# Kernel tuning notes

Hardware: AMD Instinct MI355X
Metric: run time of the kernel (lower is better)

Reference implementation:

```python
import jax, jax.numpy as jnp
import numpy as np

B, T, F = 32, 2048, 16
C = F + 1      # input channels (time prepended)
H = 64         # output_dims: latent CDE state size
HH = 64        # hidden_dims: vector-field MLP width
DEPTH = 4      # num_hidden_layers -> DEPTH-1 inner linears
INIT = 64      # intial_dims


def _lin(k, fan_in, shape):
    b = 1.0 / np.sqrt(fan_in)
    return jax.random.uniform(k, shape, jnp.float32, -b, b)


def setup_inputs() -> dict:
    key = jax.random.key(0)
    ks = jax.random.split(key, 15)
    return {
        "x": jax.random.normal(ks[0], (B, T, F), jnp.float32),
        # z0 initializer MLP: Linear(C,INIT) -> ReLU -> Linear(INIT,H)
        "wi1": _lin(ks[1], C, (C, INIT)), "bi1": _lin(ks[2], C, (INIT,)),
        "wi2": _lin(ks[3], INIT, (INIT, H)), "bi2": _lin(ks[4], INIT, (H,)),
        # CDEFunc
        "w_in": _lin(ks[5], H, (H, HH)), "b_in": _lin(ks[6], H, (HH,)),
        "w_hid": _lin(ks[7], HH, (DEPTH - 1, HH, HH)), "b_hid": _lin(ks[8], HH, (DEPTH - 1, HH)),
        "w_out": _lin(ks[9], HH, (HH, C * H)), "b_out": _lin(ks[10], HH, (C * H,)),
        # output projection Linear(H, F)
        "w_proj": _lin(ks[11], H, (H, F)), "b_proj": _lin(ks[12], H, (F,)),
    }


def _cde_f(z, w_in, b_in, w_hid, b_hid, w_out, b_out):
    # CDEFunc.forward: MLP -> tanh, reshaped to (b, H, C)
    h = jax.nn.relu(z @ w_in + b_in)
    for i in range(w_hid.shape[0]):
        h = jax.nn.relu(h @ w_hid[i] + b_hid[i])
    return jnp.tanh((h @ w_out + b_out).reshape(z.shape[0], H, C))


def _forward(x, wi1, bi1, wi2, bi2, w_in, b_in, w_hid, b_hid, w_out, b_out, w_proj, b_proj):
    b, t_len, _ = x.shape
    t = jnp.arange(t_len, dtype=x.dtype)
    xa = jnp.concatenate([jnp.broadcast_to(t[None, :, None], (b, t_len, 1)), x], axis=-1)  # (b,T,C)

    # Hermite cubic with backward differences (torchcde): knot derivs are backward
    # diffs with the first repeated; on interval i (h=1):
    #   X'(s) = d_i + 2*c_i*s + 3*e_i*s^2,  c_i = 3*dx - 2*d_i - d_{i+1},  e_i = -2*dx + d_i + d_{i+1}
    diffs = xa[:, 1:] - xa[:, :-1]                      # (b,T-1,C)
    d = jnp.concatenate([diffs[:, :1], diffs], axis=1)  # (b,T,C)
    di, dip1 = d[:, :-1], d[:, 1:]
    cc = 3.0 * diffs - 2.0 * di - dip1
    ee = -2.0 * diffs + di + dip1

    def deriv(s):
        return di + (2.0 * s) * cc + (3.0 * s * s) * ee  # (b,T-1,C)

    # torchdiffeq 'rk4' = 3/8-rule: evals at s = 0, 1/3, 2/3, 1 within each unit interval
    xdots = jnp.stack([deriv(0.0), deriv(1.0 / 3.0), deriv(2.0 / 3.0), deriv(1.0)], axis=0)
    xdots = jnp.moveaxis(xdots, 2, 0)  # (T-1, 4, b, C)

    z0 = jax.nn.relu(xa[:, 0] @ wi1 + bi1) @ wi2 + bi2  # (b,H)

    def g(z, xd):
        f = _cde_f(z, w_in, b_in, w_hid, b_hid, w_out, b_out)  # (b,H,C)
        return jnp.einsum('bhc,bc->bh', f, xd)

    def step(z, xd4):
        k1 = g(z, xd4[0])
        k2 = g(z + k1 / 3.0, xd4[1])
        k3 = g(z + (k2 - k1 / 3.0), xd4[2])
        k4 = g(z + (k1 - k2 + k3), xd4[3])
        zn = z + (k1 + 3.0 * (k2 + k3) + k4) * 0.125
        return zn, zn

    _, zs = jax.lax.scan(step, z0, xdots)                # (T-1,b,H)
    z_T = jnp.moveaxis(jnp.concatenate([z0[None], zs], axis=0), 0, 1)  # (b,T,H)

    # act -> dropout (eval: identity) -> output_layer
    out = jax.nn.gelu(z_T, approximate=False) @ w_proj + b_proj        # (b,T,F)
    return z_T, out


def reference(x, wi1, bi1, wi2, bi2, w_in, b_in, w_hid, b_hid, w_out, b_out, w_proj, b_proj):
    z_T, out = _forward(x, wi1, bi1, wi2, bi2, w_in, b_in, w_hid, b_hid, w_out, b_out, w_proj, b_proj)
    not_mask = jnp.zeros((x.shape[0], x.shape[1]), dtype=bool)  # mask='all_true' (eval mode)
    return z_T, out, not_mask
```

## Files before the change

### kernel.cpp

```cpp
#include <hip/hip_runtime.h>
#include <math.h>

#define BB 32
#define TT 2048
#define FF 16
#define CC 17
#define HH 64

typedef float v2f __attribute__((ext_vector_type(2)));
typedef float v4f __attribute__((ext_vector_type(4)));
typedef unsigned int v4u __attribute__((ext_vector_type(4)));
typedef _Float16 h2 __attribute__((ext_vector_type(2)));

__device__ __forceinline__ float rl(float v, int lane) {
    return __int_as_float(__builtin_amdgcn_readlane(__float_as_int(v), lane));
}
__device__ __forceinline__ float uf(float v) {
    return __int_as_float(__builtin_amdgcn_readfirstlane(__float_as_int(v)));
}
__device__ __forceinline__ float ftanh(float x) {
    float e = __builtin_amdgcn_exp2f(x * 2.88539008177792681472f);
    return 1.0f - 2.0f * __builtin_amdgcn_rcpf(e + 1.0f);
}
__device__ __forceinline__ float fdot2(unsigned int a, unsigned int b, float c) {
    h2 ha = __builtin_bit_cast(h2, a), hb = __builtin_bit_cast(h2, b);
#if __has_builtin(__builtin_amdgcn_fdot2)
    return __builtin_amdgcn_fdot2(ha, hb, c, false);
#else
    return fmaf((float)ha.x, (float)hb.x, fmaf((float)ha.y, (float)hb.y, c));
#endif
}
__device__ __forceinline__ unsigned int packf16(float a, float b) {
    h2 p; p.x = (_Float16)a; p.y = (_Float16)b;
    return __builtin_bit_cast(unsigned int, p);
}

#define PIN(v) asm volatile("" : "+v"(v))

__attribute__((amdgpu_waves_per_eu(2, 2)))
__launch_bounds__(512)
__global__ void ncde_main(const float* __restrict__ x,
                          const float* __restrict__ wi1, const float* __restrict__ bi1,
                          const float* __restrict__ wi2, const float* __restrict__ bi2,
                          const float* __restrict__ w_in, const float* __restrict__ b_in,
                          const float* __restrict__ w_hid, const float* __restrict__ b_hid,
                          const float* __restrict__ w_out, const float* __restrict__ b_out,
                          float* __restrict__ zT)
{
    const int b   = blockIdx.x;
    const int tid = threadIdx.x;
    const int w   = tid >> 6;
    const int l   = tid & 63;

    __shared__ float Wl[4][64][64];
    __shared__ float ph[4][8][64];
    __shared__ __align__(16) unsigned int hb16[32];
    __shared__ v2f  pgq[8][64];

    {
        float* wl = (float*)Wl;
        for (int i = tid; i < 64 * 64; i += 512)     wl[i] = w_in[i];
        for (int i = tid; i < 3 * 64 * 64; i += 512) wl[64 * 64 + i] = w_hid[i];
    }

    float bfold[4];
    bfold[0] = (w == 0) ? b_in[l] : 0.0f;
    bfold[1] = (w == 0) ? b_hid[0 * HH + l] : 0.0f;
    bfold[2] = (w == 0) ? b_hid[1 * HH + l] : 0.0f;
    bfold[3] = (w == 0) ? b_hid[2 * HH + l] : 0.0f;

    const int c0 = 2 * w, c1 = 2 * w + 1;
    unsigned int wo0p[32], wo1p[32], w16p[4];
    #pragma unroll
    for (int j = 0; j < 32; ++j) {
        wo0p[j] = packf16(w_out[(2 * j) * (CC * HH) + l * CC + c0],
                          w_out[(2 * j + 1) * (CC * HH) + l * CC + c0]);
        wo1p[j] = packf16(w_out[(2 * j) * (CC * HH) + l * CC + c1],
                          w_out[(2 * j + 1) * (CC * HH) + l * CC + c1]);
    }
    #pragma unroll
    for (int j = 0; j < 4; ++j)
        w16p[j] = packf16(w_out[(8 * w + 2 * j) * (CC * HH) + l * CC + 16],
                          w_out[(8 * w + 2 * j + 1) * (CC * HH) + l * CC + 16]);
    float bo0  = b_out[l * CC + c0];
    float bo1  = b_out[l * CC + c1];
    float bo16 = b_out[l * CC + 16];

    #pragma unroll
    for (int j = 0; j < 32; ++j) { PIN(wo0p[j]); PIN(wo1p[j]); }
    #pragma unroll
    for (int j = 0; j < 4; ++j) PIN(w16p[j]);

    __syncthreads();

    float h0 = bi1[l];
    #pragma unroll
    for (int c = 1; c < CC; ++c) {
        float xc = x[(b * TT + 0) * FF + (c - 1)];
        h0 = fmaf(xc, wi1[c * HH + l], h0);
    }
    h0 = fmaxf(h0, 0.0f);
    float z = bi2[l];
    #pragma unroll
    for (int k = 0; k < 64; ++k)
        z = fmaf(rl(h0, k), wi2[k * HH + l], z);

    if (w == 0) zT[(b * TT + 0) * HH + l] = z;

    auto G = [&](float zin, float xd0, float xd1, float xd16) -> float {
        float cur = zin;
        #pragma unroll
        for (int layer = 0; layer < 4; ++layer) {
            float wk0 = Wl[layer][8 * w + 0][l], wk1 = Wl[layer][8 * w + 1][l];
            float wk2 = Wl[layer][8 * w + 2][l], wk3 = Wl[layer][8 * w + 3][l];
            float wk4 = Wl[layer][8 * w + 4][l], wk5 = Wl[layer][8 * w + 5][l];
            float wk6 = Wl[layer][8 * w + 6][l], wk7 = Wl[layer][8 * w + 7][l];
            float a0 = bfold[layer], a1 = 0.0f;
            a0 = fmaf(rl(cur, 8 * w + 0), wk0, a0);
            a1 = fmaf(rl(cur, 8 * w + 1), wk1, a1);
            a0 = fmaf(rl(cur, 8 * w + 2), wk2, a0);
            a1 = fmaf(rl(cur, 8 * w + 3), wk3, a1);
            a0 = fmaf(rl(cur, 8 * w + 4), wk4, a0);
            a1 = fmaf(rl(cur, 8 * w + 5), wk5, a1);
            a0 = fmaf(rl(cur, 8 * w + 6), wk6, a0);
            a1 = fmaf(rl(cur, 8 * w + 7), wk7, a1);
            ph[layer][w][l] = a0 + a1;
            __syncthreads();
            float r0 = ph[layer][0][l], r1 = ph[layer][1][l];
            float r2 = ph[layer][2][l], r3 = ph[layer][3][l];
            float r4 = ph[layer][4][l], r5 = ph[layer][5][l];
            float r6 = ph[layer][6][l], r7 = ph[layer][7][l];
            cur = fmaxf(((r0 + r1) + (r2 + r3)) + ((r4 + r5) + (r6 + r7)), 0.0f);
        }
        float pm = __shfl_xor(cur, 1);
        if (w == 0 && (l & 1) == 0)
            hb16[l >> 1] = __builtin_bit_cast(unsigned int,
                __builtin_amdgcn_cvt_pkrtz(cur * 0.00390625f, pm * 0.00390625f));
        __syncthreads();

        float u0a = 0.f, u0b = 0.f, u0c = 0.f, u0d = 0.f;
        float u1a = 0.f, u1b = 0.f, u1c = 0.f, u1d = 0.f;
        #pragma unroll
        for (int j = 0; j < 8; ++j) {
            v4u q = *reinterpret_cast<const v4u*>(&hb16[4 * j]);
            u0a = fdot2(q.x, wo0p[4 * j + 0], u0a);
            u0b = fdot2(q.y, wo0p[4 * j + 1], u0b);
            u0c = fdot2(q.z, wo0p[4 * j + 2], u0c);
            u0d = fdot2(q.w, wo0p[4 * j + 3], u0d);
            u1a = fdot2(q.x, wo1p[4 * j + 0], u1a);
            u1b = fdot2(q.y, wo1p[4 * j + 1], u1b);
            u1c = fdot2(q.z, wo1p[4 * j + 2], u1c);
            u1d = fdot2(q.w, wo1p[4 * j + 3], u1d);
        }
        float u0 = fmaf(((u0a + u0b) + (u0c + u0d)), 256.0f, bo0);
        float u1 = fmaf(((u1a + u1b) + (u1c + u1d)), 256.0f, bo1);

        v4u qc = *reinterpret_cast<const v4u*>(&hb16[4 * w]);
        float a16a = fdot2(qc.x, w16p[0], 0.0f);
        float a16b = fdot2(qc.y, w16p[1], 0.0f);
        a16a = fdot2(qc.z, w16p[2], a16a);
        a16b = fdot2(qc.w, w16p[3], a16b);

        float pg = ftanh(u0) * xd0 + ftanh(u1) * xd1;
        pgq[w][l] = (v2f){ pg, a16a + a16b };
        __syncthreads();
        v2f s0 = pgq[0][l], s1 = pgq[1][l], s2 = pgq[2][l], s3 = pgq[3][l];
        v2f s4 = pgq[4][l], s5 = pgq[5][l], s6 = pgq[6][l], s7 = pgq[7][l];
        v2f st = ((s0 + s1) + (s2 + s3)) + ((s4 + s5) + (s6 + s7));
        float u16 = fmaf(st.y, 256.0f, bo16);
        return fmaf(ftanh(u16), xd16, st.x);
    };

    const float* xb = x + (size_t)b * TT * FF;
    const bool hasc0 = (w != 0);
    const int  f0 = 2 * w - 1;
    const int  f1 = 2 * w;
    float xp0  = hasc0 ? uf(xb[0 * FF + f0]) : 0.0f;
    float xp1  = uf(xb[0 * FF + f1]);
    float xp16 = uf(xb[0 * FF + 15]);
    float xn0  = hasc0 ? uf(xb[1 * FF + f0]) : 0.0f;
    float xn1  = uf(xb[1 * FF + f1]);
    float xn16 = uf(xb[1 * FF + 15]);
    float dc0  = hasc0 ? (xn0 - xp0) : 1.0f;
    float dc1  = xn1 - xp1;
    float dc16 = xn16 - xp16;
    float dp0 = dc0, dp1 = dc1, dp16 = dc16;
    xp0 = xn0; xp1 = xn1; xp16 = xn16;

    #pragma unroll 1
    for (int t = 0; t < TT - 1; ++t) {
        const float f43 = 4.0f / 3.0f;
        float x20  = dp0  + f43 * (dc0  - dp0);
        float x21  = dp1  + f43 * (dc1  - dp1);
        float x216 = dp16 + f43 * (dc16 - dp16);

        int tn = (t + 2 < TT) ? (t + 2) : (TT - 1);
        float yn0  = hasc0 ? uf(xb[tn * FF + f0]) : 0.0f;
        float yn1  = uf(xb[tn * FF + f1]);
        float yn16 = uf(xb[tn * FF + 15]);

        float k1 = G(z, dp0, dp1, dp16);
        float k2 = G(z + k1 * (1.0f / 3.0f), dc0, dc1, dc16);
        float k3 = G(z + (k2 - k1 * (1.0f / 3.0f)), x20, x21, x216);
        float k4 = G(z + (k1 - k2 + k3), dc0, dc1, dc16);
        z = z + 0.125f * (k1 + 3.0f * (k2 + k3) + k4);

        if (w == 0) zT[(b * TT + (t + 1)) * HH + l] = z;

        dp0 = dc0; dp1 = dc1; dp16 = dc16;
        dc0 = hasc0 ? (yn0 - xp0) : 1.0f;
        dc1 = yn1 - xp1;
        dc16 = yn16 - xp16;
        xp0 = yn0; xp1 = yn1; xp16 = yn16;
    }
}

__global__ void ncde_proj(const float* __restrict__ zT,
                          const float* __restrict__ w_proj, const float* __restrict__ b_proj,
                          float* __restrict__ out, float* __restrict__ mask)
{
    __shared__ float gz[16][64];
    const int blk = blockIdx.x;
    const int tid = threadIdx.x;
    const int r16 = tid >> 4, f = tid & 15;
    const int row0 = blk * 16;

    #pragma unroll
    for (int i = 0; i < 4; ++i) {
        int idx = tid + i * 256;
        int r = idx >> 6, k = idx & 63;
        float zv = zT[(size_t)(row0 + r) * HH + k];
        gz[r][k] = 0.5f * zv * (1.0f + erff(zv * 0.70710678118654752f));
    }
    __syncthreads();

    float acc = b_proj[f];
    #pragma unroll
    for (int k = 0; k < 64; ++k)
        acc = fmaf(gz[r16][k], w_proj[k * FF + f], acc);
    out[(size_t)(row0 + r16) * FF + f] = acc;
    if (f == 0) mask[row0 + r16] = 0.0f;
}

extern "C" void kernel_launch(void* const* d_in, const int* in_sizes, int n_in,
                              void* d_out, int out_size, void* d_ws, size_t ws_size,
                              hipStream_t stream)
{
    (void)in_sizes; (void)n_in; (void)d_ws; (void)ws_size; (void)out_size;
    const float* x      = (const float*)d_in[0];
    const float* wi1    = (const float*)d_in[1];
    const float* bi1    = (const float*)d_in[2];
    const float* wi2    = (const float*)d_in[3];
    const float* bi2    = (const float*)d_in[4];
    const float* w_in   = (const float*)d_in[5];
    const float* b_in   = (const float*)d_in[6];
    const float* w_hid  = (const float*)d_in[7];
    const float* b_hid  = (const float*)d_in[8];
    const float* w_out  = (const float*)d_in[9];
    const float* b_out  = (const float*)d_in[10];
    const float* w_proj = (const float*)d_in[11];
    const float* b_proj = (const float*)d_in[12];

    float* zT   = (float*)d_out;
    float* outp = zT + (size_t)BB * TT * HH;
    float* mask = outp + (size_t)BB * TT * FF;

    ncde_main<<<dim3(BB), dim3(512), 0, stream>>>(
        x, wi1, bi1, wi2, bi2, w_in, b_in, w_hid, b_hid, w_out, b_out, zT);
    ncde_proj<<<dim3((BB * TT) / 16), dim3(256), 0, stream>>>(
        zT, w_proj, b_proj, outp, mask);
}
```

Before: 14.31 ms.

## Process two batch elements per block to amortize barriers and latency

Each workgroup now integrates two independent batch sequences at once, so the grid is halved. LDS partial-sum buffers are widened so both sequences share each barrier. A lighter barrier that only waits on LDS counters replaces __syncthreads. The aim is to fill the latency and synchronisation stalls of the serial RK4 chain with independent work, at the cost of more registers and half as many active CUs.

New measurement: 21.58 ms. +50.8%, slower.

```diff
diff --git a/kernel.cpp b/kernel.cpp
--- a/kernel.cpp
+++ b/kernel.cpp
@@ -24,21 +24,18 @@
 }
 __device__ __forceinline__ float fdot2(unsigned int a, unsigned int b, float c) {
     h2 ha = __builtin_bit_cast(h2, a), hb = __builtin_bit_cast(h2, b);
-#if __has_builtin(__builtin_amdgcn_fdot2)
     return __builtin_amdgcn_fdot2(ha, hb, c, false);
-#else
-    return fmaf((float)ha.x, (float)hb.x, fmaf((float)ha.y, (float)hb.y, c));
-#endif
 }
 __device__ __forceinline__ unsigned int packf16(float a, float b) {
     h2 p; p.x = (_Float16)a; p.y = (_Float16)b;
     return __builtin_bit_cast(unsigned int, p);
 }
-
+__device__ __forceinline__ void bar_lds() {
+    asm volatile("s_waitcnt lgkmcnt(0)\n\ts_barrier" ::: "memory");
+}
 #define PIN(v) asm volatile("" : "+v"(v))
 
-__attribute__((amdgpu_waves_per_eu(2, 2)))
-__launch_bounds__(512)
+__launch_bounds__(512, 2)
 __global__ void ncde_main(const float* __restrict__ x,
                           const float* __restrict__ wi1, const float* __restrict__ bi1,
                           const float* __restrict__ wi2, const float* __restrict__ bi2,
@@ -47,15 +44,16 @@
                           const float* __restrict__ w_out, const float* __restrict__ b_out,
                           float* __restrict__ zT)
 {
-    const int b   = blockIdx.x;
+    const int bid = blockIdx.x;
+    const int eA = 2 * bid, eB = 2 * bid + 1;
     const int tid = threadIdx.x;
     const int w   = tid >> 6;
     const int l   = tid & 63;
 
     __shared__ float Wl[4][64][64];
-    __shared__ float ph[4][8][64];
-    __shared__ __align__(16) unsigned int hb16[32];
-    __shared__ v2f  pgq[8][64];
+    __shared__ v2f  ph[4][8][64];
+    __shared__ __align__(16) unsigned int hb16[64];
+    __shared__ v4f  pgq[8][64];
 
     {
         float* wl = (float*)Wl;
@@ -93,125 +91,171 @@
 
     __syncthreads();
 
-    float h0 = bi1[l];
-    #pragma unroll
-    for (int c = 1; c < CC; ++c) {
-        float xc = x[(b * TT + 0) * FF + (c - 1)];
-        h0 = fmaf(xc, wi1[c * HH + l], h0);
-    }
-    h0 = fmaxf(h0, 0.0f);
-    float z = bi2[l];
-    #pragma unroll
-    for (int k = 0; k < 64; ++k)
-        z = fmaf(rl(h0, k), wi2[k * HH + l], z);
-
-    if (w == 0) zT[(b * TT + 0) * HH + l] = z;
-
-    auto G = [&](float zin, float xd0, float xd1, float xd16) -> float {
-        float cur = zin;
+    float zA, zB;
+    {
+        float h0A = bi1[l], h0B = bi1[l];
+        #pragma unroll
+        for (int c = 1; c < CC; ++c) {
+            float w1 = wi1[c * HH + l];
+            h0A = fmaf(x[(size_t)eA * TT * FF + (c - 1)], w1, h0A);
+            h0B = fmaf(x[(size_t)eB * TT * FF + (c - 1)], w1, h0B);
+        }
+        h0A = fmaxf(h0A, 0.0f); h0B = fmaxf(h0B, 0.0f);
+        zA = bi2[l]; zB = zA;
+        #pragma unroll
+        for (int k = 0; k < 64; ++k) {
+            float w2 = wi2[k * HH + l];
+            zA = fmaf(rl(h0A, k), w2, zA);
+            zB = fmaf(rl(h0B, k), w2, zB);
+        }
+    }
+    if (w == 0) {
+        zT[(size_t)eA * TT * HH + l] = zA;
+        zT[(size_t)eB * TT * HH + l] = zB;
+    }
+
+    auto G2 = [&](float ziA, float ziB,
+                  float xa0, float xa1, float xa16,
+                  float xb0, float xb1, float xb16) -> v2f {
+        float cA = ziA, cB = ziB;
         #pragma unroll
         for (int layer = 0; layer < 4; ++layer) {
-            float wk0 = Wl[layer][8 * w + 0][l], wk1 = Wl[layer][8 * w + 1][l];
-            float wk2 = Wl[layer][8 * w + 2][l], wk3 = Wl[layer][8 * w + 3][l];
-            float wk4 = Wl[layer][8 * w + 4][l], wk5 = Wl[layer][8 * w + 5][l];
-            float wk6 = Wl[layer][8 * w + 6][l], wk7 = Wl[layer][8 * w + 7][l];
-            float a0 = bfold[layer], a1 = 0.0f;
-            a0 = fmaf(rl(cur, 8 * w + 0), wk0, a0);
-            a1 = fmaf(rl(cur, 8 * w + 1), wk1, a1);
-            a0 = fmaf(rl(cur, 8 * w + 2), wk2, a0);
-            a1 = fmaf(rl(cur, 8 * w + 3), wk3, a1);
-            a0 = fmaf(rl(cur, 8 * w + 4), wk4, a0);
-            a1 = fmaf(rl(cur, 8 * w + 5), wk5, a1);
-            a0 = fmaf(rl(cur, 8 * w + 6), wk6, a0);
-            a1 = fmaf(rl(cur, 8 * w + 7), wk7, a1);
-            ph[layer][w][l] = a0 + a1;
-            __syncthreads();
-            float r0 = ph[layer][0][l], r1 = ph[layer][1][l];
-            float r2 = ph[layer][2][l], r3 = ph[layer][3][l];
-            float r4 = ph[layer][4][l], r5 = ph[layer][5][l];
-            float r6 = ph[layer][6][l], r7 = ph[layer][7][l];
-            cur = fmaxf(((r0 + r1) + (r2 + r3)) + ((r4 + r5) + (r6 + r7)), 0.0f);
-        }
-        float pm = __shfl_xor(cur, 1);
-        if (w == 0 && (l & 1) == 0)
+            float pA  = bfold[layer], pB  = bfold[layer];
+            float pA2 = 0.0f,         pB2 = 0.0f;
+            #pragma unroll
+            for (int kk = 0; kk < 8; kk += 2) {
+                float wk0 = Wl[layer][8 * w + kk][l];
+                float wk1 = Wl[layer][8 * w + kk + 1][l];
+                float sA0 = rl(cA, 8 * w + kk), sA1 = rl(cA, 8 * w + kk + 1);
+                float sB0 = rl(cB, 8 * w + kk), sB1 = rl(cB, 8 * w + kk + 1);
+                pA  = fmaf(sA0, wk0, pA);
+                pA2 = fmaf(sA1, wk1, pA2);
+                pB  = fmaf(sB0, wk0, pB);
+                pB2 = fmaf(sB1, wk1, pB2);
+            }
+            ph[layer][w][l] = (v2f){ pA + pA2, pB + pB2 };
+            bar_lds();
+            v2f r0 = ph[layer][0][l], r1 = ph[layer][1][l];
+            v2f r2 = ph[layer][2][l], r3 = ph[layer][3][l];
+            v2f r4 = ph[layer][4][l], r5 = ph[layer][5][l];
+            v2f r6 = ph[layer][6][l], r7 = ph[layer][7][l];
+            v2f s = ((r0 + r1) + (r2 + r3)) + ((r4 + r5) + (r6 + r7));
+            cA = fmaxf(s.x, 0.0f); cB = fmaxf(s.y, 0.0f);
+        }
+        float pmA = __shfl_xor(cA, 1), pmB = __shfl_xor(cB, 1);
+        if (w == 0 && (l & 1) == 0) {
             hb16[l >> 1] = __builtin_bit_cast(unsigned int,
-                __builtin_amdgcn_cvt_pkrtz(cur * 0.00390625f, pm * 0.00390625f));
-        __syncthreads();
-
-        float u0a = 0.f, u0b = 0.f, u0c = 0.f, u0d = 0.f;
-        float u1a = 0.f, u1b = 0.f, u1c = 0.f, u1d = 0.f;
+                __builtin_amdgcn_cvt_pkrtz(cA * 0.00390625f, pmA * 0.00390625f));
+            hb16[32 + (l >> 1)] = __builtin_bit_cast(unsigned int,
+                __builtin_amdgcn_cvt_pkrtz(cB * 0.00390625f, pmB * 0.00390625f));
+        }
+        bar_lds();
+
+        float uA0a = 0.f, uA0b = 0.f, uA1a = 0.f, uA1b = 0.f;
+        float uB0a = 0.f, uB0b = 0.f, uB1a = 0.f, uB1b = 0.f;
         #pragma unroll
         for (int j = 0; j < 8; ++j) {
-            v4u q = *reinterpret_cast<const v4u*>(&hb16[4 * j]);
-            u0a = fdot2(q.x, wo0p[4 * j + 0], u0a);
-            u0b = fdot2(q.y, wo0p[4 * j + 1], u0b);
-            u0c = fdot2(q.z, wo0p[4 * j + 2], u0c);
-            u0d = fdot2(q.w, wo0p[4 * j + 3], u0d);
-            u1a = fdot2(q.x, wo1p[4 * j + 0], u1a);
-            u1b = fdot2(q.y, wo1p[4 * j + 1], u1b);
-            u1c = fdot2(q.z, wo1p[4 * j + 2], u1c);
-            u1d = fdot2(q.w, wo1p[4 * j + 3], u1d);
-        }
-        float u0 = fmaf(((u0a + u0b) + (u0c + u0d)), 256.0f, bo0);
-        float u1 = fmaf(((u1a + u1b) + (u1c + u1d)), 256.0f, bo1);
-
-        v4u qc = *reinterpret_cast<const v4u*>(&hb16[4 * w]);
-        float a16a = fdot2(qc.x, w16p[0], 0.0f);
-        float a16b = fdot2(qc.y, w16p[1], 0.0f);
-        a16a = fdot2(qc.z, w16p[2], a16a);
-        a16b = fdot2(qc.w, w16p[3], a16b);
-
-        float pg = ftanh(u0) * xd0 + ftanh(u1) * xd1;
-        pgq[w][l] = (v2f){ pg, a16a + a16b };
-        __syncthreads();
-        v2f s0 = pgq[0][l], s1 = pgq[1][l], s2 = pgq[2][l], s3 = pgq[3][l];
-        v2f s4 = pgq[4][l], s5 = pgq[5][l], s6 = pgq[6][l], s7 = pgq[7][l];
-        v2f st = ((s0 + s1) + (s2 + s3)) + ((s4 + s5) + (s6 + s7));
-        float u16 = fmaf(st.y, 256.0f, bo16);
-        return fmaf(ftanh(u16), xd16, st.x);
+            v4u qA = *reinterpret_cast<const v4u*>(&hb16[4 * j]);
+            v4u qB = *reinterpret_cast<const v4u*>(&hb16[32 + 4 * j]);
+            uA0a = fdot2(qA.x, wo0p[4 * j + 0], uA0a);
+            uA0b = fdot2(qA.y, wo0p[4 * j + 1], uA0b);
+            uA0a = fdot2(qA.z, wo0p[4 * j + 2], uA0a);
+            uA0b = fdot2(qA.w, wo0p[4 * j + 3], uA0b);
+            uA1a = fdot2(qA.x, wo1p[4 * j + 0], uA1a);
+            uA1b = fdot2(qA.y, wo1p[4 * j + 1], uA1b);
+            uA1a = fdot2(qA.z, wo1p[4 * j + 2], uA1a);
+            uA1b = fdot2(qA.w, wo1p[4 * j + 3], uA1b);
+            uB0a = fdot2(qB.x, wo0p[4 * j + 0], uB0a);
+            uB0b = fdot2(qB.y, wo0p[4 * j + 1], uB0b);
+            uB0a = fdot2(qB.z, wo0p[4 * j + 2], uB0a);
+            uB0b = fdot2(qB.w, wo0p[4 * j + 3], uB0b);
+            uB1a = fdot2(qB.x, wo1p[4 * j + 0], uB1a);
+            uB1b = fdot2(qB.y, wo1p[4 * j + 1], uB1b);
+            uB1a = fdot2(qB.z, wo1p[4 * j + 2], uB1a);
+            uB1b = fdot2(qB.w, wo1p[4 * j + 3], uB1b);
+        }
+        v4u qcA = *reinterpret_cast<const v4u*>(&hb16[4 * w]);
+        v4u qcB = *reinterpret_cast<const v4u*>(&hb16[32 + 4 * w]);
+        float aA16 = fdot2(qcA.x, w16p[0], fdot2(qcA.z, w16p[2], 0.0f));
+        float aA16b = fdot2(qcA.y, w16p[1], fdot2(qcA.w, w16p[3], 0.0f));
+        float aB16 = fdot2(qcB.x, w16p[0], fdot2(qcB.z, w16p[2], 0.0f));
+        float aB16b = fdot2(qcB.y, w16p[1], fdot2(qcB.w, w16p[3], 0.0f));
+
+        float u0A = fmaf(uA0a + uA0b, 256.0f, bo0);
+        float u1A = fmaf(uA1a + uA1b, 256.0f, bo1);
+        float u0B = fmaf(uB0a + uB0b, 256.0f, bo0);
+        float u1B = fmaf(uB1a + uB1b, 256.0f, bo1);
+        float pgA = ftanh(u0A) * xa0 + ftanh(u1A) * xa1;
+        float pgB = ftanh(u0B) * xb0 + ftanh(u1B) * xb1;
+        pgq[w][l] = (v4f){ pgA, aA16 + aA16b, pgB, aB16 + aB16b };
+        bar_lds();
+        v4f s0 = pgq[0][l], s1 = pgq[1][l], s2 = pgq[2][l], s3 = pgq[3][l];
+        v4f s4 = pgq[4][l], s5 = pgq[5][l], s6 = pgq[6][l], s7 = pgq[7][l];
+        v4f st = ((s0 + s1) + (s2 + s3)) + ((s4 + s5) + (s6 + s7));
+        float u16A = fmaf(st.y, 256.0f, bo16);
+        float u16B = fmaf(st.w, 256.0f, bo16);
+        return (v2f){ fmaf(ftanh(u16A), xa16, st.x),
+                      fmaf(ftanh(u16B), xb16, st.z) };
     };
 
-    const float* xb = x + (size_t)b * TT * FF;
+    const float* xA = x + (size_t)eA * TT * FF;
+    const float* xB = x + (size_t)eB * TT * FF;
     const bool hasc0 = (w != 0);
     const int  f0 = 2 * w - 1;
     const int  f1 = 2 * w;
-    float xp0  = hasc0 ? uf(xb[0 * FF + f0]) : 0.0f;
-    float xp1  = uf(xb[0 * FF + f1]);
-    float xp16 = uf(xb[0 * FF + 15]);
-    float xn0  = hasc0 ? uf(xb[1 * FF + f0]) : 0.0f;
-    float xn1  = uf(xb[1 * FF + f1]);
-    float xn16 = uf(xb[1 * FF + 15]);
-    float dc0  = hasc0 ? (xn0 - xp0) : 1.0f;
-    float dc1  = xn1 - xp1;
-    float dc16 = xn16 - xp16;
-    float dp0 = dc0, dp1 = dc1, dp16 = dc16;
-    xp0 = xn0; xp1 = xn1; xp16 = xn16;
+
+    float xpA0 = hasc0 ? uf(xA[f0]) : 0.0f, xpA1 = uf(xA[f1]), xpA16 = uf(xA[15]);
+    float xpB0 = hasc0 ? uf(xB[f0]) : 0.0f, xpB1 = uf(xB[f1]), xpB16 = uf(xB[15]);
+    float xnA0 = hasc0 ? uf(xA[FF + f0]) : 0.0f, xnA1 = uf(xA[FF + f1]), xnA16 = uf(xA[FF + 15]);
+    float xnB0 = hasc0 ? uf(xB[FF + f0]) : 0.0f, xnB1 = uf(xB[FF + f1]), xnB16 = uf(xB[FF + 15]);
+    float dcA0 = hasc0 ? (xnA0 - xpA0) : 1.0f, dcA1 = xnA1 - xpA1, dcA16 = xnA16 - xpA16;
+    float dcB0 = hasc0 ? (xnB0 - xpB0) : 1.0f, dcB1 = xnB1 - xpB1, dcB16 = xnB16 - xpB16;
+    float dpA0 = dcA0, dpA1 = dcA1, dpA16 = dcA16;
+    float dpB0 = dcB0, dpB1 = dcB1, dpB16 = dcB16;
+    xpA0 = xnA0; xpA1 = xnA1; xpA16 = xnA16;
+    xpB0 = xnB0; xpB1 = xnB1; xpB16 = xnB16;
 
     #pragma unroll 1
     for (int t = 0; t < TT - 1; ++t) {
         const float f43 = 4.0f / 3.0f;
-        float x20  = dp0  + f43 * (dc0  - dp0);
-        float x21  = dp1  + f43 * (dc1  - dp1);
-        float x216 = dp16 + f43 * (dc16 - dp16);
+        float x2A0 = dpA0 + f43 * (dcA0 - dpA0);
+        float x2A1 = dpA1 + f43 * (dcA1 - dpA1);
+        float x2A16 = dpA16 + f43 * (dcA16 - dpA16);
+        float x2B0 = dpB0 + f43 * (dcB0 - dpB0);
+        float x2B1 = dpB1 + f43 * (dcB1 - dpB1);
+        float x2B16 = dpB16 + f43 * (dcB16 - dpB16);
 
         int tn = (t + 2 < TT) ? (t + 2) : (TT - 1);
-        float yn0  = hasc0 ? uf(xb[tn * FF + f0]) : 0.0f;
-        float yn1  = uf(xb[tn * FF + f1]);
-        float yn16 = uf(xb[tn * FF + 15]);
-
-        float k1 = G(z, dp0, dp1, dp16);
-        float k2 = G(z + k1 * (1.0f / 3.0f), dc0, dc1, dc16);
-        float k3 = G(z + (k2 - k1 * (1.0f / 3.0f)), x20, x21, x216);
-        float k4 = G(z + (k1 - k2 + k3), dc0, dc1, dc16);
-        z = z + 0.125f * (k1 + 3.0f * (k2 + k3) + k4);
-
-        if (w == 0) zT[(b * TT + (t + 1)) * HH + l] = z;
-
-        dp0 = dc0; dp1 = dc1; dp16 = dc16;
-        dc0 = hasc0 ? (yn0 - xp0) : 1.0f;
-        dc1 = yn1 - xp1;
-        dc16 = yn16 - xp16;
-        xp0 = yn0; xp1 = yn1; xp16 = yn16;
+        float ynA0 = hasc0 ? uf(xA[tn * FF + f0]) : 0.0f;
+        float ynA1 = uf(xA[tn * FF + f1]);
+        float ynA16 = uf(xA[tn * FF + 15]);
+        float ynB0 = hasc0 ? uf(xB[tn * FF + f0]) : 0.0f;
+        float ynB1 = uf(xB[tn * FF + f1]);
+        float ynB16 = uf(xB[tn * FF + 15]);
+
+        v2f k1 = G2(zA, zB, dpA0, dpA1, dpA16, dpB0, dpB1, dpB16);
+        v2f k2 = G2(zA + k1.x * (1.0f / 3.0f), zB + k1.y * (1.0f / 3.0f),
+                    dcA0, dcA1, dcA16, dcB0, dcB1, dcB16);
+        v2f k3 = G2(zA + (k2.x - k1.x * (1.0f / 3.0f)), zB + (k2.y - k1.y * (1.0f / 3.0f)),
+                    x2A0, x2A1, x2A16, x2B0, x2B1, x2B16);
+        v2f k4 = G2(zA + (k1.x - k2.x + k3.x), zB + (k1.y - k2.y + k3.y),
+                    dcA0, dcA1, dcA16, dcB0, dcB1, dcB16);
+        zA += 0.125f * (k1.x + 3.0f * (k2.x + k3.x) + k4.x);
+        zB += 0.125f * (k1.y + 3.0f * (k2.y + k3.y) + k4.y);
+
+        if (w == 0) {
+            zT[((size_t)eA * TT + t + 1) * HH + l] = zA;
+            zT[((size_t)eB * TT + t + 1) * HH + l] = zB;
+        }
+
+        dpA0 = dcA0; dpA1 = dcA1; dpA16 = dcA16;
+        dpB0 = dcB0; dpB1 = dcB1; dpB16 = dcB16;
+        dcA0 = hasc0 ? (ynA0 - xpA0) : 1.0f;
+        dcA1 = ynA1 - xpA1; dcA16 = ynA16 - xpA16;
+        dcB0 = hasc0 ? (ynB0 - xpB0) : 1.0f;
+        dcB1 = ynB1 - xpB1; dcB16 = ynB16 - xpB16;
+        xpA0 = ynA0; xpA1 = ynA1; xpA16 = ynA16;
+        xpB0 = ynB0; xpB1 = ynB1; xpB16 = ynB16;
     }
 }
 
@@ -265,7 +309,7 @@
     float* outp = zT + (size_t)BB * TT * HH;
     float* mask = outp + (size_t)BB * TT * FF;
 
-    ncde_main<<<dim3(BB), dim3(512), 0, stream>>>(
+    ncde_main<<<dim3(BB / 2), dim3(512), 0, stream>>>(
         x, wi1, bi1, wi2, bi2, w_in, b_in, w_hid, b_hid, w_out, b_out, zT);
     ncde_proj<<<dim3((BB * TT) / 16), dim3(256), 0, stream>>>(
         zT, w_proj, b_proj, outp, mask);
```

## Compute MLP hidden layers in a single wave to cut per-layer block barriers

Applied to the files above, without the earlier changes.

The four 64x64 hidden layers now run entirely in wave 0, which reads a transposed, padded weight copy from LDS and the activation vector as broadcasts. Before, the work was split across 8 waves with a partial-sum reduction and a __syncthreads per layer. This drops four block barriers per function evaluation, and the remaining two barriers use a lighter lgkmcnt wait plus s_barrier. In exchange the layer work is serialized on one wave while the other seven sit idle. The waves_per_eu attribute is also removed and the fp16 output accumulator chains are shortened.

New measurement: 15.82 ms. 10.5% more time.

```diff
diff --git a/kernel.cpp b/kernel.cpp
--- a/kernel.cpp
+++ b/kernel.cpp
@@ -24,20 +24,13 @@
 }
 __device__ __forceinline__ float fdot2(unsigned int a, unsigned int b, float c) {
     h2 ha = __builtin_bit_cast(h2, a), hb = __builtin_bit_cast(h2, b);
-#if __has_builtin(__builtin_amdgcn_fdot2)
     return __builtin_amdgcn_fdot2(ha, hb, c, false);
-#else
-    return fmaf((float)ha.x, (float)hb.x, fmaf((float)ha.y, (float)hb.y, c));
-#endif
-}
-__device__ __forceinline__ unsigned int packf16(float a, float b) {
-    h2 p; p.x = (_Float16)a; p.y = (_Float16)b;
-    return __builtin_bit_cast(unsigned int, p);
-}
-
+}
+__device__ __forceinline__ void bar_lds() {
+    asm volatile("s_waitcnt lgkmcnt(0)\n\ts_barrier" ::: "memory");
+}
 #define PIN(v) asm volatile("" : "+v"(v))
 
-__attribute__((amdgpu_waves_per_eu(2, 2)))
 __launch_bounds__(512)
 __global__ void ncde_main(const float* __restrict__ x,
                           const float* __restrict__ wi1, const float* __restrict__ bi1,
@@ -52,36 +45,40 @@
     const int w   = tid >> 6;
     const int l   = tid & 63;
 
-    __shared__ float Wl[4][64][64];
-    __shared__ float ph[4][8][64];
+    __shared__ float WT[4 * 64 * 66];
+    __shared__ __align__(16) float hf[64];
     __shared__ __align__(16) unsigned int hb16[32];
-    __shared__ v2f  pgq[8][64];
-
-    {
-        float* wl = (float*)Wl;
-        for (int i = tid; i < 64 * 64; i += 512)     wl[i] = w_in[i];
-        for (int i = tid; i < 3 * 64 * 64; i += 512) wl[64 * 64 + i] = w_hid[i];
-    }
-
-    float bfold[4];
-    bfold[0] = (w == 0) ? b_in[l] : 0.0f;
-    bfold[1] = (w == 0) ? b_hid[0 * HH + l] : 0.0f;
-    bfold[2] = (w == 0) ? b_hid[1 * HH + l] : 0.0f;
-    bfold[3] = (w == 0) ? b_hid[2 * HH + l] : 0.0f;
+    __shared__ v2f pgq[8][64];
+
+    for (int i = tid; i < 4 * 64 * 64; i += 512) {
+        int layer = i >> 12, r = i & 4095, h = r >> 6, k = r & 63;
+        float v = (layer == 0) ? w_in[k * HH + h]
+                               : w_hid[((layer - 1) * HH + k) * HH + h];
+        WT[layer * (64 * 66) + h * 66 + k] = v;
+    }
+
+    float bh0 = b_in[l];
+    float bh1 = b_hid[0 * HH + l];
+    float bh2 = b_hid[1 * HH + l];
+    float bh3 = b_hid[2 * HH + l];
 
     const int c0 = 2 * w, c1 = 2 * w + 1;
     unsigned int wo0p[32], wo1p[32], w16p[4];
     #pragma unroll
     for (int j = 0; j < 32; ++j) {
-        wo0p[j] = packf16(w_out[(2 * j) * (CC * HH) + l * CC + c0],
-                          w_out[(2 * j + 1) * (CC * HH) + l * CC + c0]);
-        wo1p[j] = packf16(w_out[(2 * j) * (CC * HH) + l * CC + c1],
-                          w_out[(2 * j + 1) * (CC * HH) + l * CC + c1]);
-    }
-    #pragma unroll
-    for (int j = 0; j < 4; ++j)
-        w16p[j] = packf16(w_out[(8 * w + 2 * j) * (CC * HH) + l * CC + 16],
-                          w_out[(8 * w + 2 * j + 1) * (CC * HH) + l * CC + 16]);
+        h2 p0; p0.x = (_Float16)w_out[(2 * j) * (CC * HH) + l * CC + c0];
+        p0.y = (_Float16)w_out[(2 * j + 1) * (CC * HH) + l * CC + c0];
+        wo0p[j] = __builtin_bit_cast(unsigned int, p0);
+        h2 p1; p1.x = (_Float16)w_out[(2 * j) * (CC * HH) + l * CC + c1];
+        p1.y = (_Float16)w_out[(2 * j + 1) * (CC * HH) + l * CC + c1];
+        wo1p[j] = __builtin_bit_cast(unsigned int, p1);
+    }
+    #pragma unroll
+    for (int j = 0; j < 4; ++j) {
+        h2 p; p.x = (_Float16)w_out[(8 * w + 2 * j) * (CC * HH) + l * CC + 16];
+        p.y = (_Float16)w_out[(8 * w + 2 * j + 1) * (CC * HH) + l * CC + 16];
+        w16p[j] = __builtin_bit_cast(unsigned int, p);
+    }
     float bo0  = b_out[l * CC + c0];
     float bo1  = b_out[l * CC + c1];
     float bo16 = b_out[l * CC + 16];
@@ -93,77 +90,78 @@
 
     __syncthreads();
 
-    float h0 = bi1[l];
-    #pragma unroll
-    for (int c = 1; c < CC; ++c) {
-        float xc = x[(b * TT + 0) * FF + (c - 1)];
-        h0 = fmaf(xc, wi1[c * HH + l], h0);
-    }
-    h0 = fmaxf(h0, 0.0f);
-    float z = bi2[l];
-    #pragma unroll
-    for (int k = 0; k < 64; ++k)
-        z = fmaf(rl(h0, k), wi2[k * HH + l], z);
-
-    if (w == 0) zT[(b * TT + 0) * HH + l] = z;
+    float z;
+    {
+        float h0 = bi1[l];
+        #pragma unroll
+        for (int c = 1; c < CC; ++c)
+            h0 = fmaf(x[(size_t)b * TT * FF + (c - 1)], wi1[c * HH + l], h0);
+        h0 = fmaxf(h0, 0.0f);
+        z = bi2[l];
+        #pragma unroll
+        for (int k = 0; k < 64; ++k)
+            z = fmaf(rl(h0, k), wi2[k * HH + l], z);
+    }
+    if (w == 7) zT[(size_t)b * TT * HH + l] = z;
 
     auto G = [&](float zin, float xd0, float xd1, float xd16) -> float {
-        float cur = zin;
-        #pragma unroll
-        for (int layer = 0; layer < 4; ++layer) {
-            float wk0 = Wl[layer][8 * w + 0][l], wk1 = Wl[layer][8 * w + 1][l];
-            float wk2 = Wl[layer][8 * w + 2][l], wk3 = Wl[layer][8 * w + 3][l];
-            float wk4 = Wl[layer][8 * w + 4][l], wk5 = Wl[layer][8 * w + 5][l];
-            float wk6 = Wl[layer][8 * w + 6][l], wk7 = Wl[layer][8 * w + 7][l];
-            float a0 = bfold[layer], a1 = 0.0f;
-            a0 = fmaf(rl(cur, 8 * w + 0), wk0, a0);
-            a1 = fmaf(rl(cur, 8 * w + 1), wk1, a1);
-            a0 = fmaf(rl(cur, 8 * w + 2), wk2, a0);
-            a1 = fmaf(rl(cur, 8 * w + 3), wk3, a1);
-            a0 = fmaf(rl(cur, 8 * w + 4), wk4, a0);
-            a1 = fmaf(rl(cur, 8 * w + 5), wk5, a1);
-            a0 = fmaf(rl(cur, 8 * w + 6), wk6, a0);
-            a1 = fmaf(rl(cur, 8 * w + 7), wk7, a1);
-            ph[layer][w][l] = a0 + a1;
-            __syncthreads();
-            float r0 = ph[layer][0][l], r1 = ph[layer][1][l];
-            float r2 = ph[layer][2][l], r3 = ph[layer][3][l];
-            float r4 = ph[layer][4][l], r5 = ph[layer][5][l];
-            float r6 = ph[layer][6][l], r7 = ph[layer][7][l];
-            cur = fmaxf(((r0 + r1) + (r2 + r3)) + ((r4 + r5) + (r6 + r7)), 0.0f);
+        if (w == 0) {
+            hf[l] = zin;
+            float cur;
+            #pragma unroll
+            for (int layer = 0; layer < 4; ++layer) {
+                const float* WL = &WT[layer * (64 * 66) + l * 66];
+                v2f a0 = { 0.f, 0.f }, a1 = { 0.f, 0.f };
+                v2f a2 = { 0.f, 0.f }, a3 = { 0.f, 0.f };
+                #pragma unroll
+                for (int jj = 0; jj < 16; jj += 2) {
+                    v4f q0 = *reinterpret_cast<const v4f*>(&hf[4 * jj]);
+                    v4f q1 = *reinterpret_cast<const v4f*>(&hf[4 * jj + 4]);
+                    v2f w00 = *reinterpret_cast<const v2f*>(&WL[4 * jj]);
+                    v2f w01 = *reinterpret_cast<const v2f*>(&WL[4 * jj + 2]);
+                    v2f w10 = *reinterpret_cast<const v2f*>(&WL[4 * jj + 4]);
+                    v2f w11 = *reinterpret_cast<const v2f*>(&WL[4 * jj + 6]);
+                    a0 += w00 * (v2f){ q0.x, q0.y };
+                    a1 += w01 * (v2f){ q0.z, q0.w };
+                    a2 += w10 * (v2f){ q1.x, q1.y };
+                    a3 += w11 * (v2f){ q1.z, q1.w };
+                }
+                v2f s = (a0 + a1) + (a2 + a3);
+                float bias = (layer == 0) ? bh0 : (layer == 1) ? bh1 : (layer == 2) ? bh2 : bh3;
+                cur = fmaxf(s.x + s.y + bias, 0.0f);
+                if (layer < 3) hf[l] = cur;
+            }
+            float sc = cur * 0.00390625f;
+            float ot = __shfl_xor(sc, 1);
+            if ((l & 1) == 0)
+                hb16[l >> 1] = __builtin_bit_cast(unsigned int,
+                    __builtin_amdgcn_cvt_pkrtz(sc, ot));
         }
-        float pm = __shfl_xor(cur, 1);
-        if (w == 0 && (l & 1) == 0)
-            hb16[l >> 1] = __builtin_bit_cast(unsigned int,
-                __builtin_amdgcn_cvt_pkrtz(cur * 0.00390625f, pm * 0.00390625f));
-        __syncthreads();
-
-        float u0a = 0.f, u0b = 0.f, u0c = 0.f, u0d = 0.f;
-        float u1a = 0.f, u1b = 0.f, u1c = 0.f, u1d = 0.f;
+        bar_lds();
+
+        float u0a = 0.f, u0b = 0.f, u1a = 0.f, u1b = 0.f;
         #pragma unroll
         for (int j = 0; j < 8; ++j) {
             v4u q = *reinterpret_cast<const v4u*>(&hb16[4 * j]);
             u0a = fdot2(q.x, wo0p[4 * j + 0], u0a);
             u0b = fdot2(q.y, wo0p[4 * j + 1], u0b);
-            u0c = fdot2(q.z, wo0p[4 * j + 2], u0c);
-            u0d = fdot2(q.w, wo0p[4 * j + 3], u0d);
+            u0a = fdot2(q.z, wo0p[4 * j + 2], u0a);
+            u0b = fdot2(q.w, wo0p[4 * j + 3], u0b);
             u1a = fdot2(q.x, wo1p[4 * j + 0], u1a);
             u1b = fdot2(q.y, wo1p[4 * j + 1], u1b);
-            u1c = fdot2(q.z, wo1p[4 * j + 2], u1c);
-            u1d = fdot2(q.w, wo1p[4 * j + 3], u1d);
+            u1a = fdot2(q.z, wo1p[4 * j + 2], u1a);
+            u1b = fdot2(q.w, wo1p[4 * j + 3], u1b);
         }
-        float u0 = fmaf(((u0a + u0b) + (u0c + u0d)), 256.0f, bo0);
-        float u1 = fmaf(((u1a + u1b) + (u1c + u1d)), 256.0f, bo1);
-
         v4u qc = *reinterpret_cast<const v4u*>(&hb16[4 * w]);
-        float a16a = fdot2(qc.x, w16p[0], 0.0f);
-        float a16b = fdot2(qc.y, w16p[1], 0.0f);
-        a16a = fdot2(qc.z, w16p[2], a16a);
-        a16b = fdot2(qc.w, w16p[3], a16b);
-
+        float a16a = fdot2(qc.x, w16p[0], fdot2(qc.z, w16p[2], 0.0f));
+        float a16b = fdot2(qc.y, w16p[1], fdot2(qc.w, w16p[3], 0.0f));
+
+        float u0 = fmaf(u0a + u0b, 256.0f, bo0);
+        float u1 = fmaf(u1a + u1b, 256.0f, bo1);
         float pg = ftanh(u0) * xd0 + ftanh(u1) * xd1;
         pgq[w][l] = (v2f){ pg, a16a + a16b };
-        __syncthreads();
+        bar_lds();
+
         v2f s0 = pgq[0][l], s1 = pgq[1][l], s2 = pgq[2][l], s3 = pgq[3][l];
         v2f s4 = pgq[4][l], s5 = pgq[5][l], s6 = pgq[6][l], s7 = pgq[7][l];
         v2f st = ((s0 + s1) + (s2 + s3)) + ((s4 + s5) + (s6 + s7));
@@ -175,12 +173,12 @@
     const bool hasc0 = (w != 0);
     const int  f0 = 2 * w - 1;
     const int  f1 = 2 * w;
-    float xp0  = hasc0 ? uf(xb[0 * FF + f0]) : 0.0f;
-    float xp1  = uf(xb[0 * FF + f1]);
-    float xp16 = uf(xb[0 * FF + 15]);
-    float xn0  = hasc0 ? uf(xb[1 * FF + f0]) : 0.0f;
-    float xn1  = uf(xb[1 * FF + f1]);
-    float xn16 = uf(xb[1 * FF + 15]);
+    float xp0  = hasc0 ? uf(xb[f0]) : 0.0f;
+    float xp1  = uf(xb[f1]);
+    float xp16 = uf(xb[15]);
+    float xn0  = hasc0 ? uf(xb[FF + f0]) : 0.0f;
+    float xn1  = uf(xb[FF + f1]);
+    float xn16 = uf(xb[FF + 15]);
     float dc0  = hasc0 ? (xn0 - xp0) : 1.0f;
     float dc1  = xn1 - xp1;
     float dc16 = xn16 - xp16;
@@ -205,7 +203,7 @@
         float k4 = G(z + (k1 - k2 + k3), dc0, dc1, dc16);
         z = z + 0.125f * (k1 + 3.0f * (k2 + k3) + k4);
 
-        if (w == 0) zT[(b * TT + (t + 1)) * HH + l] = z;
+        if (w == 7) zT[((size_t)b * TT + t + 1) * HH + l] = z;
 
         dp0 = dc0; dp1 = dc1; dp16 = dc16;
         dc0 = hasc0 ? (yn0 - xp0) : 1.0f;
```
